# Kernel optimization log

Hardware: AMD Instinct MI355X
Metric: run time of the kernel (lower is better)

## Reference

```python
import jax, jax.numpy as jnp
import numpy as np

IGNORE_INDEX = -100


def setup_inputs() -> dict:
    key = jax.random.key(0)
    ks = jax.random.split(key, 12)
    B, NS, S, H, WE, L = 32, 4096, 512, 768, 150, 9
    return {
        "sequence_output": jax.random.normal(ks[0], (B, S, H), jnp.float32),
        "width_table": jax.random.normal(ks[1], (9, WE), jnp.float32),
        "W1": jax.random.normal(ks[2], (2 * H + WE, WE), jnp.float32) * 0.02,
        "b1": jax.random.normal(ks[3], (WE,), jnp.float32) * 0.02,
        "W2": jax.random.normal(ks[4], (WE, WE), jnp.float32) * 0.02,
        "b2": jax.random.normal(ks[5], (WE,), jnp.float32) * 0.02,
        "W3": jax.random.normal(ks[6], (WE, L), jnp.float32) * 0.02,
        "b3": jax.random.normal(ks[7], (L,), jnp.float32) * 0.02,
        "spans": jax.random.randint(ks[8], (B, NS, 3), 0, 9).astype(jnp.int64),
        "spans_mask": jax.random.randint(ks[9], (B, NS), 0, 2).astype(jnp.int64),
        "spans_ner_label": jax.random.randint(ks[10], (B, NS), 0, 9).astype(jnp.int64),
    }


def reference(sequence_output, width_table, W1, b1, W2, b2, W3, b3,
              spans, spans_mask, spans_ner_label):
    # spans: [B, NS, 3] -> (start, end, width)
    start = spans[:, :, 0]  # [B, NS]
    end = spans[:, :, 1]
    width = spans[:, :, 2]
    # One-hot @ sequence_output in the torch code == exact gather of token reps.
    start_rep = jnp.take_along_axis(sequence_output, start[:, :, None], axis=1)  # [B, NS, H]
    end_rep = jnp.take_along_axis(sequence_output, end[:, :, None], axis=1)      # [B, NS, H]
    width_rep = width_table[width]                                               # [B, NS, WE]
    rep = jnp.concatenate([start_rep, end_rep, width_rep], axis=-1)              # [B, NS, 2H+WE]
    # final_layer: ReLU -> Linear -> (Dropout) -> ReLU -> Linear -> (Dropout) -> Linear
    h = jax.nn.relu(rep)
    h = jax.nn.relu(h @ W1 + b1)
    h = h @ W2 + b2
    logits = h @ W3 + b3                                                         # [B, NS, L]
    # CrossEntropyLoss(reduction='sum') with ignore_index on inactive spans
    flat_logits = logits.reshape(-1, logits.shape[-1])
    active = spans_mask.reshape(-1) == 1
    labels = jnp.where(active, spans_ner_label.reshape(-1), IGNORE_INDEX)
    logp = jax.nn.log_softmax(flat_logits, axis=-1)
    safe = jnp.clip(labels, 0, logits.shape[-1] - 1)
    picked = jnp.take_along_axis(logp, safe[:, None], axis=1)[:, 0]
    loss = -jnp.sum(jnp.where(labels >= 0, picked, 0.0))
    return logits, loss
```

## Files before the change

### kernel.cpp

```cpp
#include <hip/hip_runtime.h>
#include <math.h>

#define NB 32
#define SEQ 512
#define HD 768
#define NL 9
#define NSPAN (NB * 4096)
#define LOGITS_N (NSPAN * NL)
#define RS 156

template <int CH>
__global__ __launch_bounds__(320) void stageA(
    const float* __restrict__ seq, const float* __restrict__ wtab,
    const float* __restrict__ W1, const float* __restrict__ b1,
    const float* __restrict__ W2, const float* __restrict__ b2,
    const float* __restrict__ W3, const float* __restrict__ b3,
    float* __restrict__ part, float* __restrict__ wwt,
    float* __restrict__ w23p, float* __restrict__ b23p,
    float* __restrict__ out)
{
  constexpr int CK = 768 / CH;
  const int gid = blockIdx.x, t = threadIdx.x;

  if (gid < 32 * CH) {
    __shared__ __align__(16) float xr[9 * CK];
    const int b = gid / CH, chunk = gid - b * CH;
    const float* sb = seq + (size_t)b * SEQ * HD + chunk * CK;
    for (int i = t; i < 9 * CK; i += 320) {
      int s = i / CK, k = i - s * CK;
      xr[i] = fmaxf(sb[(size_t)s * HD + k], 0.f);
    }
    __syncthreads();
    if (t < 300) {
      const int half = t / 150, j = t - 150 * half;
      float acc[9];
#pragma unroll
      for (int s = 0; s < 9; ++s) acc[s] = 0.f;
      const float* w1p = W1 + (size_t)(half * 768 + chunk * CK) * 150 + j;
      for (int k = 0; k < CK; k += 4) {
        float wv0 = w1p[(size_t)(k + 0) * 150];
        float wv1 = w1p[(size_t)(k + 1) * 150];
        float wv2 = w1p[(size_t)(k + 2) * 150];
        float wv3 = w1p[(size_t)(k + 3) * 150];
#pragma unroll
        for (int s = 0; s < 9; ++s) {
          const float4 x = *(const float4*)&xr[s * CK + k];
          acc[s] = fmaf(x.x, wv0, fmaf(x.y, wv1, fmaf(x.z, wv2, fmaf(x.w, wv3, acc[s]))));
        }
      }
      float* op = part + ((size_t)gid * 2 + half) * 1350 + j;
#pragma unroll
      for (int s = 0; s < 9; ++s) op[s * 150] = acc[s];
    }
  } else if (gid < 32 * CH + 9) {
    __shared__ float xw[152];
    const int w = gid - 32 * CH;
    for (int i = t; i < 150; i += 320) xw[i] = fmaxf(wtab[w * 150 + i], 0.f);
    __syncthreads();
    if (t < 150) {
      const int j = t;
      float a = b1[j];
      const float* wp = W1 + (size_t)1536 * 150 + j;
#pragma unroll 3
      for (int k = 0; k < 150; k += 2) {
        a = fmaf(xw[k], wp[(size_t)k * 150], a);
        a = fmaf(xw[k + 1], wp[(size_t)(k + 1) * 150], a);
      }
      wwt[w * 150 + j] = a;
    }
  } else {
    __shared__ float w3l[1350];
    const int o = (gid - 32 * CH - 9) * 320 + t;
    for (int i = t; i < 1350; i += 320) w3l[i] = W3[i];
    __syncthreads();
    if (o < 1350) {
      const int j = o / 9, l = o - 9 * j;
      const float2* w2p = (const float2*)(W2 + (size_t)j * 150);
      float a = 0.f;
#pragma unroll 5
      for (int m = 0; m < 75; ++m) {
        float2 v = w2p[m];
        a = fmaf(v.x, w3l[(2 * m) * 9 + l], a);
        a = fmaf(v.y, w3l[(2 * m + 1) * 9 + l], a);
      }
      w23p[j * 12 + l] = a;
    } else if (o < 1359) {
      const int l = o - 1350;
      float a = b3[l];
#pragma unroll 5
      for (int m = 0; m < 150; ++m) a = fmaf(b2[m], w3l[m * 9 + l], a);
      b23p[l] = a;
    }
    if (gid == 32 * CH + 9 && t == 0) out[LOGITS_N] = 0.f;
  }
}

template <int CH>
__global__ __launch_bounds__(256) void stageB(
    const float* __restrict__ part, const float* __restrict__ wwt,
    const float* __restrict__ w23p, const float* __restrict__ b23p,
    float* __restrict__ ctab)
{
  __shared__ __align__(16) float swl[9 * RS];
  __shared__ __align__(16) float ewl[9 * RS];
  __shared__ __align__(16) float wwl[9 * RS];
  __shared__ __align__(16) float w23l[1800];
  __shared__ float b23l[12];

  const int t = threadIdx.x, blk = blockIdx.x;
  const int b = blk / 6, q = blk - 6 * b;
  const float* pb = part + (size_t)b * CH * 2700;
  for (int o = t; o < 1350; o += 256) {
    float vs = 0.f, ve = 0.f;
#pragma unroll
    for (int c2 = 0; c2 < CH; ++c2) {
      vs += pb[c2 * 2700 + o];
      ve += pb[c2 * 2700 + 1350 + o];
    }
    const int s = o / 150, j = o - 150 * s;
    swl[s * RS + j] = vs;
    ewl[s * RS + j] = ve;
    wwl[s * RS + j] = wwt[o];
  }
  for (int o = t; o < 1800; o += 256) w23l[o] = w23p[o];
  if (t < 9) b23l[t] = b23p[t];
  __syncthreads();

  const int c = q * 128 + t;
  if (t >= 128 || c >= 729) return;
  const int s = c / 81, r0 = c - 81 * s, e = r0 / 9, w = r0 - 9 * e;
  const float* Ap = swl + s * RS;
  const float* Bp = ewl + e * RS;
  const float* Cp = wwl + w * RS;

  float acc[9];
#pragma unroll
  for (int l = 0; l < 9; ++l) acc[l] = b23l[l];

  for (int j = 0; j < 148; j += 4) {
    float4 a = *(const float4*)(Ap + j);
    float4 d = *(const float4*)(Bp + j);
    float4 cc = *(const float4*)(Cp + j);
    float h[4];
    h[0] = fmaxf(a.x + d.x + cc.x, 0.f);
    h[1] = fmaxf(a.y + d.y + cc.y, 0.f);
    h[2] = fmaxf(a.z + d.z + cc.z, 0.f);
    h[3] = fmaxf(a.w + d.w + cc.w, 0.f);
#pragma unroll
    for (int rr = 0; rr < 4; ++rr) {
      const float* wr = w23l + (j + rr) * 12;
      float4 wa = *(const float4*)(wr);
      float4 wb = *(const float4*)(wr + 4);
      float wc = wr[8];
      float p = h[rr];
      acc[0] = fmaf(p, wa.x, acc[0]);
      acc[1] = fmaf(p, wa.y, acc[1]);
      acc[2] = fmaf(p, wa.z, acc[2]);
      acc[3] = fmaf(p, wa.w, acc[3]);
      acc[4] = fmaf(p, wb.x, acc[4]);
      acc[5] = fmaf(p, wb.y, acc[5]);
      acc[6] = fmaf(p, wb.z, acc[6]);
      acc[7] = fmaf(p, wb.w, acc[7]);
      acc[8] = fmaf(p, wc, acc[8]);
    }
  }
#pragma unroll
  for (int j = 148; j < 150; ++j) {
    float p = fmaxf(Ap[j] + Bp[j] + Cp[j], 0.f);
    const float* wr = w23l + j * 12;
#pragma unroll
    for (int l = 0; l < 9; ++l) acc[l] = fmaf(p, wr[l], acc[l]);
  }

  float m = acc[0];
#pragma unroll
  for (int l = 1; l < 9; ++l) m = fmaxf(m, acc[l]);
  float ssum = 0.f;
#pragma unroll
  for (int l = 0; l < 9; ++l) ssum += __expf(acc[l] - m);
  const float lse = m + __logf(ssum);

  float* op = ctab + (size_t)(b * 729 + c) * 12;
  *(float4*)(op) = make_float4(acc[0], acc[1], acc[2], acc[3]);
  *(float4*)(op + 4) = make_float4(acc[4], acc[5], acc[6], acc[7]);
  *(float2*)(op + 8) = make_float2(acc[8], lse);
}

__global__ __launch_bounds__(128) void stageC(
    const float* __restrict__ ctab, const int* __restrict__ spans,
    const int* __restrict__ mask, const int* __restrict__ label,
    float* __restrict__ out)
{
  __shared__ __align__(16) float ctl[729 * 12];
  __shared__ float red[2];
  const int t = threadIdx.x, blk = blockIdx.x;
  const int b = blk >> 3;

  const float4* src = (const float4*)(ctab + (size_t)b * 729 * 12);
  float4* dst = (float4*)ctl;
  for (int i = t; i < 2187; i += 128) dst[i] = src[i];
  __syncthreads();

  const int i0 = blk * 512 + t * 4;
  const int4* sp = (const int4*)(spans + (size_t)3 * i0);
  const int4 sp0 = sp[0], sp1 = sp[1], sp2 = sp[2];
  const int4 mk = *(const int4*)(mask + i0);
  const int4 lb = *(const int4*)(label + i0);
  const int ss[4] = {sp0.x, sp0.w, sp1.z, sp2.y};
  const int ee[4] = {sp0.y, sp1.x, sp1.w, sp2.z};
  const int wws[4] = {sp0.z, sp1.y, sp2.x, sp2.w};
  const int mks[4] = {mk.x, mk.y, mk.z, mk.w};
  const int lbs[4] = {lb.x, lb.y, lb.z, lb.w};

  float buf[36];
  float loss = 0.f;
#pragma unroll
  for (int u = 0; u < 4; ++u) {
    const int s = min(max(ss[u], 0), 8);
    const int e = min(max(ee[u], 0), 8);
    const int w = min(max(wws[u], 0), 8);
    const int base = ((s * 9 + e) * 9 + w) * 12;
    const float4 v0 = *(const float4*)&ctl[base];
    const float4 v1 = *(const float4*)&ctl[base + 4];
    const float2 v2 = *(const float2*)&ctl[base + 8];
    buf[u * 9 + 0] = v0.x; buf[u * 9 + 1] = v0.y; buf[u * 9 + 2] = v0.z;
    buf[u * 9 + 3] = v0.w; buf[u * 9 + 4] = v1.x; buf[u * 9 + 5] = v1.y;
    buf[u * 9 + 6] = v1.z; buf[u * 9 + 7] = v1.w; buf[u * 9 + 8] = v2.x;
    if (mks[u] == 1) {
      const int l = min(max(lbs[u], 0), 8);
      float p = v0.x;
      p = (l == 1) ? v0.y : p;
      p = (l == 2) ? v0.z : p;
      p = (l == 3) ? v0.w : p;
      p = (l == 4) ? v1.x : p;
      p = (l == 5) ? v1.y : p;
      p = (l == 6) ? v1.z : p;
      p = (l == 7) ? v1.w : p;
      p = (l == 8) ? v2.x : p;
      loss += v2.y - p;
    }
  }
  float4* op = (float4*)(out + (size_t)i0 * 9);
#pragma unroll
  for (int r = 0; r < 9; ++r)
    op[r] = make_float4(buf[4 * r], buf[4 * r + 1], buf[4 * r + 2], buf[4 * r + 3]);

#pragma unroll
  for (int off = 32; off > 0; off >>= 1) loss += __shfl_down(loss, off);
  if ((t & 63) == 0) red[t >> 6] = loss;
  __syncthreads();
  if (t == 0) atomicAdd(out + LOGITS_N, red[0] + red[1]);
}

extern "C" void kernel_launch(void* const* d_in, const int* in_sizes, int n_in,
                              void* d_out, int out_size, void* d_ws, size_t ws_size,
                              hipStream_t stream) {
  const float* seq  = (const float*)d_in[0];
  const float* wtab = (const float*)d_in[1];
  const float* W1   = (const float*)d_in[2];
  const float* b1   = (const float*)d_in[3];
  const float* W2   = (const float*)d_in[4];
  const float* b2   = (const float*)d_in[5];
  const float* W3   = (const float*)d_in[6];
  const float* b3   = (const float*)d_in[7];
  const int* spans  = (const int*)d_in[8];
  const int* mask   = (const int*)d_in[9];
  const int* label  = (const int*)d_in[10];
  float* out = (float*)d_out;
  float* ws  = (float*)d_ws;
  (void)in_sizes; (void)n_in; (void)out_size;

  const size_t tail = 1352 + 1800 + 16 + (size_t)32 * 729 * 12;
  const size_t cap = ws_size / 4;
  int CH = 1;
  if (cap >= (size_t)32 * 16 * 2700 + tail) CH = 16;
  else if (cap >= (size_t)32 * 8 * 2700 + tail) CH = 8;
  else if (cap >= (size_t)32 * 4 * 2700 + tail) CH = 4;
  else if (cap >= (size_t)32 * 2 * 2700 + tail) CH = 2;

  float* part = ws;
  float* wwt  = ws + (size_t)32 * CH * 2700;
  float* w23p = wwt + 1352;
  float* b23p = w23p + 1800;
  float* ctab = b23p + 16;

  switch (CH) {
    case 16:
      stageA<16><<<32 * 16 + 15, 320, 0, stream>>>(seq, wtab, W1, b1, W2, b2, W3, b3, part, wwt, w23p, b23p, out);
      stageB<16><<<192, 256, 0, stream>>>(part, wwt, w23p, b23p, ctab);
      break;
    case 8:
      stageA<8><<<32 * 8 + 15, 320, 0, stream>>>(seq, wtab, W1, b1, W2, b2, W3, b3, part, wwt, w23p, b23p, out);
      stageB<8><<<192, 256, 0, stream>>>(part, wwt, w23p, b23p, ctab);
      break;
    case 4:
      stageA<4><<<32 * 4 + 15, 320, 0, stream>>>(seq, wtab, W1, b1, W2, b2, W3, b3, part, wwt, w23p, b23p, out);
      stageB<4><<<192, 256, 0, stream>>>(part, wwt, w23p, b23p, ctab);
      break;
    case 2:
      stageA<2><<<32 * 2 + 15, 320, 0, stream>>>(seq, wtab, W1, b1, W2, b2, W3, b3, part, wwt, w23p, b23p, out);
      stageB<2><<<192, 256, 0, stream>>>(part, wwt, w23p, b23p, ctab);
      break;
    default:
      stageA<1><<<32 * 1 + 15, 320, 0, stream>>>(seq, wtab, W1, b1, W2, b2, W3, b3, part, wwt, w23p, b23p, out);
      stageB<1><<<192, 256, 0, stream>>>(part, wwt, w23p, b23p, ctab);
      break;
  }
  stageC<<<256, 128, 0, stream>>>(ctab, spans, mask, label, out);
}
```

Before: 133.5 us.

## Fuse combo-table and span-gather stages into one per-span kernel, fix CH=8

Drops the precomputed 729-entry combination table. A single kernel now rebuilds the per-batch start, end and width tables in shared memory and runs the 150x9 projection for every span directly (131k spans instead of 23k combos), then writes logits and the loss in the same pass. Stage A no longer stages the relu'd rows in LDS; each thread reads the sequence rows directly, and the chunk count is hardwired to 8. This saves one launch and the ctab round trip. In exchange it does about 5.6x more FLOPs, each of 512 blocks re-reduces the partials, and w23 is read from global memory instead of LDS.

Result: slower. 145.7 us (+9.1%).

```diff
diff --git a/kernel.cpp b/kernel.cpp
--- a/kernel.cpp
+++ b/kernel.cpp
@@ -8,8 +8,10 @@
 #define NSPAN (NB * 4096)
 #define LOGITS_N (NSPAN * NL)
 #define RS 156
-
-template <int CH>
+#define CH 8
+#define CK 96
+
+
 __global__ __launch_bounds__(320) void stageA(
     const float* __restrict__ seq, const float* __restrict__ wtab,
     const float* __restrict__ W1, const float* __restrict__ b1,
@@ -19,42 +21,41 @@
     float* __restrict__ w23p, float* __restrict__ b23p,
     float* __restrict__ out)
 {
-  constexpr int CK = 768 / CH;
   const int gid = blockIdx.x, t = threadIdx.x;
 
-  if (gid < 32 * CH) {
-    __shared__ __align__(16) float xr[9 * CK];
-    const int b = gid / CH, chunk = gid - b * CH;
+  if (gid < 256) {
+    if (t >= 300) return;
+    const int b = gid >> 3, chunk = gid & 7;
+    const int half = t / 150, j = t - 150 * half;
     const float* sb = seq + (size_t)b * SEQ * HD + chunk * CK;
-    for (int i = t; i < 9 * CK; i += 320) {
-      int s = i / CK, k = i - s * CK;
-      xr[i] = fmaxf(sb[(size_t)s * HD + k], 0.f);
-    }
-    __syncthreads();
-    if (t < 300) {
-      const int half = t / 150, j = t - 150 * half;
-      float acc[9];
-#pragma unroll
-      for (int s = 0; s < 9; ++s) acc[s] = 0.f;
-      const float* w1p = W1 + (size_t)(half * 768 + chunk * CK) * 150 + j;
-      for (int k = 0; k < CK; k += 4) {
-        float wv0 = w1p[(size_t)(k + 0) * 150];
-        float wv1 = w1p[(size_t)(k + 1) * 150];
-        float wv2 = w1p[(size_t)(k + 2) * 150];
-        float wv3 = w1p[(size_t)(k + 3) * 150];
-#pragma unroll
-        for (int s = 0; s < 9; ++s) {
-          const float4 x = *(const float4*)&xr[s * CK + k];
-          acc[s] = fmaf(x.x, wv0, fmaf(x.y, wv1, fmaf(x.z, wv2, fmaf(x.w, wv3, acc[s]))));
-        }
+    const float* w1p = W1 + (size_t)(half * 768 + chunk * CK) * 150 + j;
+    float acc[9];
+#pragma unroll
+    for (int s = 0; s < 9; ++s) acc[s] = 0.f;
+    for (int k = 0; k < CK; k += 4) {
+      float4 xv[9];
+#pragma unroll
+      for (int s = 0; s < 9; ++s) xv[s] = *(const float4*)(sb + (size_t)s * HD + k);
+      const float wv0 = w1p[(size_t)(k + 0) * 150];
+      const float wv1 = w1p[(size_t)(k + 1) * 150];
+      const float wv2 = w1p[(size_t)(k + 2) * 150];
+      const float wv3 = w1p[(size_t)(k + 3) * 150];
+#pragma unroll
+      for (int s = 0; s < 9; ++s) {
+        float a = acc[s];
+        a = fmaf(fmaxf(xv[s].x, 0.f), wv0, a);
+        a = fmaf(fmaxf(xv[s].y, 0.f), wv1, a);
+        a = fmaf(fmaxf(xv[s].z, 0.f), wv2, a);
+        a = fmaf(fmaxf(xv[s].w, 0.f), wv3, a);
+        acc[s] = a;
       }
-      float* op = part + ((size_t)gid * 2 + half) * 1350 + j;
-#pragma unroll
-      for (int s = 0; s < 9; ++s) op[s * 150] = acc[s];
-    }
-  } else if (gid < 32 * CH + 9) {
+    }
+    float* op = part + ((size_t)gid * 2 + half) * 1350 + j;
+#pragma unroll
+    for (int s = 0; s < 9; ++s) op[s * 150] = acc[s];
+  } else if (gid < 265) {
     __shared__ float xw[152];
-    const int w = gid - 32 * CH;
+    const int w = gid - 256;
     for (int i = t; i < 150; i += 320) xw[i] = fmaxf(wtab[w * 150 + i], 0.f);
     __syncthreads();
     if (t < 150) {
@@ -70,7 +71,7 @@
     }
   } else {
     __shared__ float w3l[1350];
-    const int o = (gid - 32 * CH - 9) * 320 + t;
+    const int o = (gid - 265) * 320 + t;
     for (int i = t; i < 1350; i += 320) w3l[i] = W3[i];
     __syncthreads();
     if (o < 1350) {
@@ -91,51 +92,49 @@
       for (int m = 0; m < 150; ++m) a = fmaf(b2[m], w3l[m * 9 + l], a);
       b23p[l] = a;
     }
-    if (gid == 32 * CH + 9 && t == 0) out[LOGITS_N] = 0.f;
+    if (gid == 265 && t == 0) out[LOGITS_N] = 0.f;
   }
 }
 
-template <int CH>
-__global__ __launch_bounds__(256) void stageB(
+__global__ __launch_bounds__(256) void spanK(
     const float* __restrict__ part, const float* __restrict__ wwt,
     const float* __restrict__ w23p, const float* __restrict__ b23p,
-    float* __restrict__ ctab)
+    const int* __restrict__ spans, const int* __restrict__ mask,
+    const int* __restrict__ label, float* __restrict__ out)
 {
   __shared__ __align__(16) float swl[9 * RS];
   __shared__ __align__(16) float ewl[9 * RS];
   __shared__ __align__(16) float wwl[9 * RS];
-  __shared__ __align__(16) float w23l[1800];
-  __shared__ float b23l[12];
+  __shared__ float red[4];
 
   const int t = threadIdx.x, blk = blockIdx.x;
-  const int b = blk / 6, q = blk - 6 * b;
-  const float* pb = part + (size_t)b * CH * 2700;
+  const int b = blk >> 4;
+
+  const float* pb = part + (size_t)b * 8 * 2700;
   for (int o = t; o < 1350; o += 256) {
     float vs = 0.f, ve = 0.f;
 #pragma unroll
-    for (int c2 = 0; c2 < CH; ++c2) {
-      vs += pb[c2 * 2700 + o];
-      ve += pb[c2 * 2700 + 1350 + o];
+    for (int c = 0; c < 8; ++c) {
+      vs += pb[c * 2700 + o];
+      ve += pb[c * 2700 + 1350 + o];
     }
     const int s = o / 150, j = o - 150 * s;
     swl[s * RS + j] = vs;
     ewl[s * RS + j] = ve;
     wwl[s * RS + j] = wwt[o];
   }
-  for (int o = t; o < 1800; o += 256) w23l[o] = w23p[o];
-  if (t < 9) b23l[t] = b23p[t];
   __syncthreads();
 
-  const int c = q * 128 + t;
-  if (t >= 128 || c >= 729) return;
-  const int s = c / 81, r0 = c - 81 * s, e = r0 / 9, w = r0 - 9 * e;
-  const float* Ap = swl + s * RS;
-  const float* Bp = ewl + e * RS;
-  const float* Cp = wwl + w * RS;
+  const int i0 = blk * 256 + t;
+  int s0 = spans[3 * i0 + 0], e0 = spans[3 * i0 + 1], w0 = spans[3 * i0 + 2];
+  s0 = min(max(s0, 0), 8); e0 = min(max(e0, 0), 8); w0 = min(max(w0, 0), 8);
+  const float* Ap = swl + s0 * RS;
+  const float* Bp = ewl + e0 * RS;
+  const float* Cp = wwl + w0 * RS;
 
   float acc[9];
 #pragma unroll
-  for (int l = 0; l < 9; ++l) acc[l] = b23l[l];
+  for (int l = 0; l < 9; ++l) acc[l] = b23p[l];
 
   for (int j = 0; j < 148; j += 4) {
     float4 a = *(const float4*)(Ap + j);
@@ -147,12 +146,12 @@
     h[2] = fmaxf(a.z + d.z + cc.z, 0.f);
     h[3] = fmaxf(a.w + d.w + cc.w, 0.f);
 #pragma unroll
-    for (int rr = 0; rr < 4; ++rr) {
-      const float* wr = w23l + (j + rr) * 12;
-      float4 wa = *(const float4*)(wr);
-      float4 wb = *(const float4*)(wr + 4);
-      float wc = wr[8];
-      float p = h[rr];
+    for (int r = 0; r < 4; ++r) {
+      const float* wr = w23p + (j + r) * 12;
+      const float4 wa = *(const float4*)(wr);
+      const float4 wb = *(const float4*)(wr + 4);
+      const float wc = wr[8];
+      const float p = h[r];
       acc[0] = fmaf(p, wa.x, acc[0]);
       acc[1] = fmaf(p, wa.y, acc[1]);
       acc[2] = fmaf(p, wa.z, acc[2]);
@@ -166,8 +165,8 @@
   }
 #pragma unroll
   for (int j = 148; j < 150; ++j) {
-    float p = fmaxf(Ap[j] + Bp[j] + Cp[j], 0.f);
-    const float* wr = w23l + j * 12;
+    const float p = fmaxf(Ap[j] + Bp[j] + Cp[j], 0.f);
+    const float* wr = w23p + j * 12;
 #pragma unroll
     for (int l = 0; l < 9; ++l) acc[l] = fmaf(p, wr[l], acc[l]);
   }
@@ -180,76 +179,24 @@
   for (int l = 0; l < 9; ++l) ssum += __expf(acc[l] - m);
   const float lse = m + __logf(ssum);
 
-  float* op = ctab + (size_t)(b * 729 + c) * 12;
-  *(float4*)(op) = make_float4(acc[0], acc[1], acc[2], acc[3]);
-  *(float4*)(op + 4) = make_float4(acc[4], acc[5], acc[6], acc[7]);
-  *(float2*)(op + 8) = make_float2(acc[8], lse);
-}
-
-__global__ __launch_bounds__(128) void stageC(
-    const float* __restrict__ ctab, const int* __restrict__ spans,
-    const int* __restrict__ mask, const int* __restrict__ label,
-    float* __restrict__ out)
-{
-  __shared__ __align__(16) float ctl[729 * 12];
-  __shared__ float red[2];
-  const int t = threadIdx.x, blk = blockIdx.x;
-  const int b = blk >> 3;
-
-  const float4* src = (const float4*)(ctab + (size_t)b * 729 * 12);
-  float4* dst = (float4*)ctl;
-  for (int i = t; i < 2187; i += 128) dst[i] = src[i];
-  __syncthreads();
-
-  const int i0 = blk * 512 + t * 4;
-  const int4* sp = (const int4*)(spans + (size_t)3 * i0);
-  const int4 sp0 = sp[0], sp1 = sp[1], sp2 = sp[2];
-  const int4 mk = *(const int4*)(mask + i0);
-  const int4 lb = *(const int4*)(label + i0);
-  const int ss[4] = {sp0.x, sp0.w, sp1.z, sp2.y};
-  const int ee[4] = {sp0.y, sp1.x, sp1.w, sp2.z};
-  const int wws[4] = {sp0.z, sp1.y, sp2.x, sp2.w};
-  const int mks[4] = {mk.x, mk.y, mk.z, mk.w};
-  const int lbs[4] = {lb.x, lb.y, lb.z, lb.w};
-
-  float buf[36];
+  float* op = out + (size_t)i0 * 9;
+#pragma unroll
+  for (int l = 0; l < 9; ++l) op[l] = acc[l];
+
   float loss = 0.f;
-#pragma unroll
-  for (int u = 0; u < 4; ++u) {
-    const int s = min(max(ss[u], 0), 8);
-    const int e = min(max(ee[u], 0), 8);
-    const int w = min(max(wws[u], 0), 8);
-    const int base = ((s * 9 + e) * 9 + w) * 12;
-    const float4 v0 = *(const float4*)&ctl[base];
-    const float4 v1 = *(const float4*)&ctl[base + 4];
-    const float2 v2 = *(const float2*)&ctl[base + 8];
-    buf[u * 9 + 0] = v0.x; buf[u * 9 + 1] = v0.y; buf[u * 9 + 2] = v0.z;
-    buf[u * 9 + 3] = v0.w; buf[u * 9 + 4] = v1.x; buf[u * 9 + 5] = v1.y;
-    buf[u * 9 + 6] = v1.z; buf[u * 9 + 7] = v1.w; buf[u * 9 + 8] = v2.x;
-    if (mks[u] == 1) {
-      const int l = min(max(lbs[u], 0), 8);
-      float p = v0.x;
-      p = (l == 1) ? v0.y : p;
-      p = (l == 2) ? v0.z : p;
-      p = (l == 3) ? v0.w : p;
-      p = (l == 4) ? v1.x : p;
-      p = (l == 5) ? v1.y : p;
-      p = (l == 6) ? v1.z : p;
-      p = (l == 7) ? v1.w : p;
-      p = (l == 8) ? v2.x : p;
-      loss += v2.y - p;
-    }
-  }
-  float4* op = (float4*)(out + (size_t)i0 * 9);
-#pragma unroll
-  for (int r = 0; r < 9; ++r)
-    op[r] = make_float4(buf[4 * r], buf[4 * r + 1], buf[4 * r + 2], buf[4 * r + 3]);
-
+  if (mask[i0] == 1) {
+    const int lb = min(max(label[i0], 0), 8);
+    float picked = acc[0];
+#pragma unroll
+    for (int l = 1; l < 9; ++l) picked = (lb == l) ? acc[l] : picked;
+    loss = lse - picked;
+  }
 #pragma unroll
   for (int off = 32; off > 0; off >>= 1) loss += __shfl_down(loss, off);
   if ((t & 63) == 0) red[t >> 6] = loss;
   __syncthreads();
-  if (t == 0) atomicAdd(out + LOGITS_N, red[0] + red[1]);
+  if (t == 0)
+    atomicAdd(out + LOGITS_N, (red[0] + red[1]) + (red[2] + red[3]));
 }
 
 extern "C" void kernel_launch(void* const* d_in, const int* in_sizes, int n_in,
@@ -268,43 +215,15 @@
   const int* label  = (const int*)d_in[10];
   float* out = (float*)d_out;
   float* ws  = (float*)d_ws;
-  (void)in_sizes; (void)n_in; (void)out_size;
-
-  const size_t tail = 1352 + 1800 + 16 + (size_t)32 * 729 * 12;
-  const size_t cap = ws_size / 4;
-  int CH = 1;
-  if (cap >= (size_t)32 * 16 * 2700 + tail) CH = 16;
-  else if (cap >= (size_t)32 * 8 * 2700 + tail) CH = 8;
-  else if (cap >= (size_t)32 * 4 * 2700 + tail) CH = 4;
-  else if (cap >= (size_t)32 * 2 * 2700 + tail) CH = 2;
+  (void)in_sizes; (void)n_in; (void)out_size; (void)ws_size;
 
   float* part = ws;
-  float* wwt  = ws + (size_t)32 * CH * 2700;
+  float* wwt  = ws + (size_t)32 * 8 * 2700;
   float* w23p = wwt + 1352;
   float* b23p = w23p + 1800;
-  float* ctab = b23p + 16;
-
-  switch (CH) {
-    case 16:
-      stageA<16><<<32 * 16 + 15, 320, 0, stream>>>(seq, wtab, W1, b1, W2, b2, W3, b3, part, wwt, w23p, b23p, out);
-      stageB<16><<<192, 256, 0, stream>>>(part, wwt, w23p, b23p, ctab);
-      break;
-    case 8:
-      stageA<8><<<32 * 8 + 15, 320, 0, stream>>>(seq, wtab, W1, b1, W2, b2, W3, b3, part, wwt, w23p, b23p, out);
-      stageB<8><<<192, 256, 0, stream>>>(part, wwt, w23p, b23p, ctab);
-      break;
-    case 4:
-      stageA<4><<<32 * 4 + 15, 320, 0, stream>>>(seq, wtab, W1, b1, W2, b2, W3, b3, part, wwt, w23p, b23p, out);
-      stageB<4><<<192, 256, 0, stream>>>(part, wwt, w23p, b23p, ctab);
-      break;
-    case 2:
-      stageA<2><<<32 * 2 + 15, 320, 0, stream>>>(seq, wtab, W1, b1, W2, b2, W3, b3, part, wwt, w23p, b23p, out);
-      stageB<2><<<192, 256, 0, stream>>>(part, wwt, w23p, b23p, ctab);
-      break;
-    default:
-      stageA<1><<<32 * 1 + 15, 320, 0, stream>>>(seq, wtab, W1, b1, W2, b2, W3, b3, part, wwt, w23p, b23p, out);
-      stageB<1><<<192, 256, 0, stream>>>(part, wwt, w23p, b23p, ctab);
-      break;
-  }
-  stageC<<<256, 128, 0, stream>>>(ctab, spans, mask, label, out);
+
+  stageA<<<271, 320, 0, stream>>>(seq, wtab, W1, b1, W2, b2, W3, b3,
+                                  part, wwt, w23p, b23p, out);
+  spanK<<<512, 256, 0, stream>>>(part, wwt, w23p, b23p,
+                                 spans, mask, label, out);
 }
```
